# Kernel tuning notes

Measured on AMD Instinct MI355X. Metric: run time of the kernel, lower is better.

The kernel has to match this reference:

```python
import jax, jax.numpy as jnp
import numpy as np

H_MODEL = 1024
N_HEADS = 16
N_KV_HEADS = 4
HEAD_DIM = 64
SLIDING_WINDOW = 512
B, S = 2, 2048
NEG_INF = -1e9


def rotate_half(x):
    half = x.shape[-1] // 2
    return jnp.concatenate([-x[..., half:], x[..., :half]], axis=-1)


def setup_inputs() -> dict:
    key = jax.random.key(0)
    ks = jax.random.split(key, 8)
    hidden_states = jax.random.normal(ks[0], (B, S, H_MODEL), dtype=jnp.float32)
    # RoPE tables (HF style): cos/sin of shape [1, S, head_dim]
    inv_freq = 1.0 / (10000.0 ** (jnp.arange(0, HEAD_DIM, 2, dtype=jnp.float32) / HEAD_DIM))
    pos = jnp.arange(S, dtype=jnp.float32)
    freqs = jnp.einsum('s,d->sd', pos, inv_freq)            # [S, D/2]
    emb = jnp.concatenate([freqs, freqs], axis=-1)          # [S, D]
    cos = jnp.cos(emb)[None]                                # [1, S, D]
    sin = jnp.sin(emb)[None]
    # additive causal + sliding-window mask [1,1,S,S]
    i = jnp.arange(S)[:, None]
    j = jnp.arange(S)[None, :]
    allowed = (j <= i) & (i - j < SLIDING_WINDOW)
    attention_mask = jnp.where(allowed, 0.0, NEG_INF).astype(jnp.float32)[None, None]
    # projection weights (torch Linear stores [out, in]; y = x @ W.T)
    std = 0.02
    Wq = jax.random.normal(ks[1], (N_HEADS * HEAD_DIM, H_MODEL), dtype=jnp.float32) * std
    Wk = jax.random.normal(ks[2], (N_KV_HEADS * HEAD_DIM, H_MODEL), dtype=jnp.float32) * std
    Wv = jax.random.normal(ks[3], (N_KV_HEADS * HEAD_DIM, H_MODEL), dtype=jnp.float32) * std
    Wo = jax.random.normal(ks[4], (H_MODEL, N_HEADS * HEAD_DIM), dtype=jnp.float32) * std
    return {"hidden_states": hidden_states, "cos": cos, "sin": sin,
            "attention_mask": attention_mask, "Wq": Wq, "Wk": Wk, "Wv": Wv, "Wo": Wo}


def reference(hidden_states, cos, sin, attention_mask, Wq, Wk, Wv, Wo):
    b, s, _ = hidden_states.shape
    G = N_HEADS // N_KV_HEADS
    scaling = HEAD_DIM ** -0.5
    # QKV projections -> [B, H, S, D]
    q = jnp.einsum('bsh,oh->bso', hidden_states, Wq).reshape(b, s, N_HEADS, HEAD_DIM).transpose(0, 2, 1, 3)
    k = jnp.einsum('bsh,oh->bso', hidden_states, Wk).reshape(b, s, N_KV_HEADS, HEAD_DIM).transpose(0, 2, 1, 3)
    v = jnp.einsum('bsh,oh->bso', hidden_states, Wv).reshape(b, s, N_KV_HEADS, HEAD_DIM).transpose(0, 2, 1, 3)
    # RoPE (cos/sin broadcast over head dim via unsqueeze(1))
    c = cos[:, None, :, :]
    sn = sin[:, None, :, :]
    q = q * c + rotate_half(q) * sn
    k = k * c + rotate_half(k) * sn
    # GQA eager attention: group query heads over kv heads
    qg = q.reshape(b, N_KV_HEADS, G, s, HEAD_DIM)
    scores = jnp.einsum('bkgqd,bkpd->bkgqp', qg, k) * scaling  # [B,Hkv,G,S,S]
    scores = scores + attention_mask[:, :, None, :, :]
    probs = jax.nn.softmax(scores.astype(jnp.float32), axis=-1).astype(q.dtype)
    out = jnp.einsum('bkgqp,bkpd->bkgqd', probs, v)            # [B,Hkv,G,S,D]
    out = out.reshape(b, N_HEADS, s, HEAD_DIM).transpose(0, 2, 1, 3).reshape(b, s, N_HEADS * HEAD_DIM)
    return jnp.einsum('bso,ho->bsh', out, Wo)
```

## Files before the change

kernel.cpp:

```cpp
#include <hip/hip_runtime.h>
#include <hip/hip_bf16.h>

#define S_LEN 2048
#define NH 16
#define NKV 4
#define HD 64
#define WIN 512
#define BATCH 2

typedef __bf16 bf16_8 __attribute__((ext_vector_type(8)));
typedef __bf16 bf16_4 __attribute__((ext_vector_type(4)));
typedef float f32x4 __attribute__((ext_vector_type(4)));

__device__ inline void gld16(const __bf16* g, __bf16* l) {
    __builtin_amdgcn_global_load_lds(
        (const __attribute__((address_space(1))) void*)g,
        (__attribute__((address_space(3))) void*)l, 16, 0, 0);
}

__global__ __launch_bounds__(256) void cvt5(
    const float* __restrict__ s0, const float* __restrict__ s1,
    const float* __restrict__ s2, const float* __restrict__ s3,
    const float* __restrict__ s4,
    __bf16* __restrict__ d0, __bf16* __restrict__ d1,
    __bf16* __restrict__ d2, __bf16* __restrict__ d3,
    __bf16* __restrict__ d4,
    int c0, int c1, int c2, int c3, int c4)
{
    const int i = blockIdx.x * blockDim.x + threadIdx.x;
    if (i >= c4) return;
    const float* s; __bf16* d; int base;
    if (i < c0)      { s = s0; d = d0; base = 0;  }
    else if (i < c1) { s = s1; d = d1; base = c0; }
    else if (i < c2) { s = s2; d = d2; base = c1; }
    else if (i < c3) { s = s3; d = d3; base = c2; }
    else             { s = s4; d = d4; base = c3; }
    const size_t j = (size_t)(i - base) * 4;
    const f32x4 v = *(const f32x4*)(s + j);
    bf16_4 o;
    o[0] = (__bf16)v[0]; o[1] = (__bf16)v[1];
    o[2] = (__bf16)v[2]; o[3] = (__bf16)v[3];
    *(bf16_4*)(d + j) = o;
}

__global__ __launch_bounds__(256) void gemm_qkv(
    const __bf16* __restrict__ A,
    const __bf16* __restrict__ Wqb,
    const __bf16* __restrict__ Wkb,
    const __bf16* __restrict__ Wvb,
    __bf16* __restrict__ Qb,
    __bf16* __restrict__ Kb,
    __bf16* __restrict__ Vb,
    const float* __restrict__ cosb,
    const float* __restrict__ sinb)
{
    const int K = 1024;
    __shared__ __align__(16) __bf16 As[128 * 32];
    __shared__ __align__(16) __bf16 Bs[128 * 32];

    const int tid  = threadIdx.x;
    const int wave = tid >> 6;
    const int lane = tid & 63;
    const int wr   = wave >> 1;
    const int wc   = wave & 1;

    const int row0 = blockIdx.x * 128;
    const int by   = blockIdx.y;

    const __bf16* B; __bf16* C; int ldc; int col0; bool rope;
    if (by < 8)       { B = Wqb + (size_t)by * 128 * K;        C = Qb; ldc = 1024; col0 = by * 128;        rope = true;  }
    else if (by < 10) { B = Wkb + (size_t)(by - 8) * 128 * K;  C = Kb; ldc = 256;  col0 = (by - 8) * 128;  rope = true;  }
    else              { B = Wvb + (size_t)(by - 10) * 128 * K; C = Vb; ldc = 256;  col0 = (by - 10) * 128; rope = false; }

    const int srow = lane >> 2;
    const int skc  = (lane & 3) << 3;

    const int fm = lane & 15;
    const int fk = (lane >> 4) << 3;

    const f32x4 fzero = {0.f, 0.f, 0.f, 0.f};
    f32x4 acc[4][4];
#pragma unroll
    for (int i = 0; i < 4; ++i)
#pragma unroll
        for (int nt = 0; nt < 4; ++nt) acc[i][nt] = fzero;

    const int ra0 = wave * 16 + srow;
    const int ra1 = 64 + wave * 16 + srow;

    for (int k0 = 0; k0 < K; k0 += 32) {
        gld16(&A[(size_t)(row0 + ra0) * K + k0 + skc], &As[(wave * 16) * 32]);
        gld16(&A[(size_t)(row0 + ra1) * K + k0 + skc], &As[(64 + wave * 16) * 32]);
        gld16(&B[(size_t)ra0 * K + k0 + skc],          &Bs[(wave * 16) * 32]);
        gld16(&B[(size_t)ra1 * K + k0 + skc],          &Bs[(64 + wave * 16) * 32]);
        __syncthreads();

        bf16_8 af[4], bf[4];
#pragma unroll
        for (int i = 0; i < 4; ++i)
            af[i] = *(const bf16_8*)&As[(wr * 64 + i * 16 + fm) * 32 + fk];
#pragma unroll
        for (int nt = 0; nt < 4; ++nt)
            bf[nt] = *(const bf16_8*)&Bs[(wc * 64 + nt * 16 + fm) * 32 + fk];
#pragma unroll
        for (int i = 0; i < 4; ++i)
#pragma unroll
            for (int nt = 0; nt < 4; ++nt)
                acc[i][nt] = __builtin_amdgcn_mfma_f32_16x16x32_bf16(af[i], bf[nt], acc[i][nt], 0, 0, 0);
        __syncthreads();
    }

    const int drow = (lane >> 4) << 2;
    const int cq   = col0 + wc * 64;
#pragma unroll
    for (int i = 0; i < 4; ++i) {
#pragma unroll
        for (int r = 0; r < 4; ++r) {
            const int row = row0 + wr * 64 + i * 16 + drow + r;
            const int s   = row & (S_LEN - 1);
            if (rope) {
#pragma unroll
                for (int nt = 0; nt < 2; ++nt) {
                    const int d = nt * 16 + fm;
                    const float c1 = cosb[s * HD + d];
                    const float s1 = sinb[s * HD + d];
                    const float c2 = cosb[s * HD + d + 32];
                    const float s2 = sinb[s * HD + d + 32];
                    const float x1 = acc[i][nt][r];
                    const float x2 = acc[i][nt + 2][r];
                    C[(size_t)row * ldc + cq + d]      = (__bf16)(x1 * c1 - x2 * s1);
                    C[(size_t)row * ldc + cq + d + 32] = (__bf16)(x2 * c2 + x1 * s2);
                }
            } else {
#pragma unroll
                for (int nt = 0; nt < 4; ++nt)
                    C[(size_t)row * ldc + cq + nt * 16 + fm] = (__bf16)acc[i][nt][r];
            }
        }
    }
}

__global__ __launch_bounds__(256) void gemm_o(
    const __bf16* __restrict__ A,
    const __bf16* __restrict__ B,
    float* __restrict__ C)
{
    const int K = 1024;
    __shared__ __align__(16) __bf16 As[128 * 32];
    __shared__ __align__(16) __bf16 Bs[128 * 32];

    const int tid  = threadIdx.x;
    const int wave = tid >> 6;
    const int lane = tid & 63;
    const int wr   = wave >> 1;
    const int wc   = wave & 1;

    const int row0 = blockIdx.x * 128;
    const int col0 = blockIdx.y * 128;

    const int srow = lane >> 2;
    const int skc  = (lane & 3) << 3;
    const int fm = lane & 15;
    const int fk = (lane >> 4) << 3;

    const f32x4 fzero = {0.f, 0.f, 0.f, 0.f};
    f32x4 acc[4][4];
#pragma unroll
    for (int i = 0; i < 4; ++i)
#pragma unroll
        for (int nt = 0; nt < 4; ++nt) acc[i][nt] = fzero;

    const int ra0 = wave * 16 + srow;
    const int ra1 = 64 + wave * 16 + srow;

    for (int k0 = 0; k0 < K; k0 += 32) {
        gld16(&A[(size_t)(row0 + ra0) * K + k0 + skc], &As[(wave * 16) * 32]);
        gld16(&A[(size_t)(row0 + ra1) * K + k0 + skc], &As[(64 + wave * 16) * 32]);
        gld16(&B[(size_t)(col0 + ra0) * K + k0 + skc], &Bs[(wave * 16) * 32]);
        gld16(&B[(size_t)(col0 + ra1) * K + k0 + skc], &Bs[(64 + wave * 16) * 32]);
        __syncthreads();

        bf16_8 af[4], bf[4];
#pragma unroll
        for (int i = 0; i < 4; ++i)
            af[i] = *(const bf16_8*)&As[(wr * 64 + i * 16 + fm) * 32 + fk];
#pragma unroll
        for (int nt = 0; nt < 4; ++nt)
            bf[nt] = *(const bf16_8*)&Bs[(wc * 64 + nt * 16 + fm) * 32 + fk];
#pragma unroll
        for (int i = 0; i < 4; ++i)
#pragma unroll
            for (int nt = 0; nt < 4; ++nt)
                acc[i][nt] = __builtin_amdgcn_mfma_f32_16x16x32_bf16(af[i], bf[nt], acc[i][nt], 0, 0, 0);
        __syncthreads();
    }

    const int drow = (lane >> 4) << 2;
#pragma unroll
    for (int i = 0; i < 4; ++i)
#pragma unroll
        for (int r = 0; r < 4; ++r) {
            const int row = row0 + wr * 64 + i * 16 + drow + r;
#pragma unroll
            for (int nt = 0; nt < 4; ++nt)
                C[(size_t)row * 1024 + col0 + wc * 64 + nt * 16 + fm] = acc[i][nt][r];
        }
}

__global__ __launch_bounds__(256) void attn_mfma(const __bf16* __restrict__ Q,
                                                 const __bf16* __restrict__ K,
                                                 const __bf16* __restrict__ V,
                                                 __bf16* __restrict__ O)
{
    __shared__ __align__(16) __bf16 Vt[HD][40];
    __shared__ __align__(16) __bf16 Ps[4][16][40];

    const int tid  = threadIdx.x;
    const int wave = tid >> 6;
    const int lane = tid & 63;

    const int qt = blockIdx.x & (S_LEN / 64 - 1);
    const int h  = (blockIdx.x >> 5) & (NH - 1);
    const int b  = blockIdx.x >> 9;
    const int kh = h >> 2;

    const int q0 = qt * 64;
    const int qw = q0 + wave * 16;

    const int fm = lane & 15;
    const int fj = (lane >> 4) << 3;

    const size_t qrow = (size_t)(b * S_LEN + qw + fm) * (NH * HD) + h * HD;
    const bf16_8 qf0 = *(const bf16_8*)&Q[qrow + fj];
    const bf16_8 qf1 = *(const bf16_8*)&Q[qrow + 32 + fj];

    const f32x4 fzero = {0.f, 0.f, 0.f, 0.f};
    f32x4 oacc[4];
    float l[4];
#pragma unroll
    for (int nt = 0; nt < 4; ++nt) oacc[nt] = fzero;
#pragma unroll
    for (int r = 0; r < 4; ++r) l[r] = 0.f;

    const int sj = tid & 31;
    const int sd = (tid >> 5) << 3;

    const int kb_lo = (q0 >= WIN) ? (q0 - WIN) : 0;
    const int qbase = qw + ((lane >> 4) << 2);

    for (int kb = kb_lo; kb <= q0 + 63; kb += 32) {
        __syncthreads();
        {
            bf16_8 vrow = *(const bf16_8*)&V[(size_t)(b * S_LEN + kb + sj) * (NKV * HD) + kh * HD + sd];
#pragma unroll
            for (int u = 0; u < 8; ++u) Vt[sd + u][sj] = vrow[u];
        }
        __syncthreads();

        if (kb <= qw + 15 && (qw - kb) < (WIN + 31)) {
            f32x4 s0 = fzero, s1 = fzero;
            {
                const size_t kr0 = (size_t)(b * S_LEN + kb + fm) * (NKV * HD) + kh * HD;
                const size_t kr1 = (size_t)(b * S_LEN + kb + 16 + fm) * (NKV * HD) + kh * HD;
                bf16_8 k00 = *(const bf16_8*)&K[kr0 + fj];
                bf16_8 k01 = *(const bf16_8*)&K[kr0 + 32 + fj];
                bf16_8 k10 = *(const bf16_8*)&K[kr1 + fj];
                bf16_8 k11 = *(const bf16_8*)&K[kr1 + 32 + fj];
                s0 = __builtin_amdgcn_mfma_f32_16x16x32_bf16(qf0, k00, s0, 0, 0, 0);
                s0 = __builtin_amdgcn_mfma_f32_16x16x32_bf16(qf1, k01, s0, 0, 0, 0);
                s1 = __builtin_amdgcn_mfma_f32_16x16x32_bf16(qf0, k10, s1, 0, 0, 0);
                s1 = __builtin_amdgcn_mfma_f32_16x16x32_bf16(qf1, k11, s1, 0, 0, 0);
            }

            float p0[4], p1[4];
            const int k0i = kb + fm;
            const int k1i = kb + 16 + fm;
#pragma unroll
            for (int r = 0; r < 4; ++r) {
                const int qr = qbase + r;
                const float e0 = __expf(s0[r] * 0.125f);
                const float e1 = __expf(s1[r] * 0.125f);
                p0[r] = (k0i <= qr && qr - k0i < WIN) ? e0 : 0.f;
                p1[r] = (k1i <= qr && qr - k1i < WIN) ? e1 : 0.f;
                l[r] += p0[r] + p1[r];
            }

#pragma unroll
            for (int r = 0; r < 4; ++r) {
                Ps[wave][((lane >> 4) << 2) + r][fm]      = (__bf16)p0[r];
                Ps[wave][((lane >> 4) << 2) + r][16 + fm] = (__bf16)p1[r];
            }

            const bf16_8 pf = *(const bf16_8*)&Ps[wave][fm][fj];
#pragma unroll
            for (int nt = 0; nt < 4; ++nt) {
                const bf16_8 vf = *(const bf16_8*)&Vt[nt * 16 + fm][fj];
                oacc[nt] = __builtin_amdgcn_mfma_f32_16x16x32_bf16(pf, vf, oacc[nt], 0, 0, 0);
            }
        }
    }

#pragma unroll
    for (int off = 8; off > 0; off >>= 1)
#pragma unroll
        for (int r = 0; r < 4; ++r)
            l[r] += __shfl_xor(l[r], off, 64);

    const int drow = (lane >> 4) << 2;
    float inv[4];
#pragma unroll
    for (int r = 0; r < 4; ++r) inv[r] = 1.0f / l[r];
#pragma unroll
    for (int nt = 0; nt < 4; ++nt)
#pragma unroll
        for (int r = 0; r < 4; ++r) {
            const size_t off = (size_t)(b * S_LEN + qw + drow + r) * (NH * HD) + h * HD + nt * 16 + fm;
            O[off] = (__bf16)(oacc[nt][r] * inv[r]);
        }
}

extern "C" void kernel_launch(void* const* d_in, const int* in_sizes, int n_in,
                              void* d_out, int out_size, void* d_ws, size_t ws_size,
                              hipStream_t stream)
{
    const float* hs   = (const float*)d_in[0];
    const float* cosb = (const float*)d_in[1];
    const float* sinb = (const float*)d_in[2];
    const float* Wq = (const float*)d_in[4];
    const float* Wk = (const float*)d_in[5];
    const float* Wv = (const float*)d_in[6];
    const float* Wo = (const float*)d_in[7];

    const int M = BATCH * S_LEN;

    __bf16* hsb = (__bf16*)d_ws;
    __bf16* Ob  = hsb;
    __bf16* Wqb = hsb + (size_t)M * 1024;
    __bf16* Wkb = Wqb + 1024 * 1024;
    __bf16* Wvb = Wkb + 256 * 1024;
    __bf16* Wob = Wvb + 256 * 1024;
    __bf16* Qb  = Wob + 1024 * 1024;
    __bf16* Kb  = Qb  + (size_t)M * 1024;
    __bf16* Vb  = Kb  + (size_t)M * 256;

    const int c0 = 1048576;
    const int c1 = c0 + 262144;
    const int c2 = c1 + 65536;
    const int c3 = c2 + 65536;
    const int c4 = c3 + 262144;

    dim3 blk(256);
    cvt5<<<(c4 + 255) / 256, blk, 0, stream>>>(hs, Wq, Wk, Wv, Wo,
                                               hsb, Wqb, Wkb, Wvb, Wob,
                                               c0, c1, c2, c3, c4);

    gemm_qkv<<<dim3(32, 12), blk, 0, stream>>>(hsb, Wqb, Wkb, Wvb,
                                               Qb, Kb, Vb, cosb, sinb);

    attn_mfma<<<BATCH * NH * (S_LEN / 64), blk, 0, stream>>>(Qb, Kb, Vb, Ob);

    gemm_o<<<dim3(32, 8), blk, 0, stream>>>(Ob, Wob, (float*)d_out);
}
```

Measured before the change: 188.9 us.

## Pre-transpose V in QKV GEMM, drop attention LDS staging, shrink GEMM tiles

The QKV GEMM epilogue now writes V directly in a transposed [b,kv,d,s] layout. The attention kernel then reads V fragments straight from global memory instead of staging and transposing them through shared memory with two block barriers per key step. Each wave also iterates only over its own window-limited key range instead of the block-wide range. The GEMMs switch to 64x128 tiles via a shared macro, doubling grid size for better CU coverage at the cost of less per-block reuse and strided scattered V stores.

```diff
diff --git a/kernel.cpp b/kernel.cpp
--- a/kernel.cpp
+++ b/kernel.cpp
@@ -43,6 +43,47 @@
     *(bf16_4*)(d + j) = o;
 }
 
+#define GEMM_BODY(A_, B_, row0_, colb_)                                        \
+    __shared__ __align__(16) __bf16 As[64 * 32];                               \
+    __shared__ __align__(16) __bf16 Bs[128 * 32];                              \
+    const int tid  = threadIdx.x;                                              \
+    const int wave = tid >> 6;                                                 \
+    const int lane = tid & 63;                                                 \
+    const int wm   = wave & 1;                                                 \
+    const int wn   = wave >> 1;                                                \
+    const int srow = lane >> 2;                                                \
+    const int skc  = (lane & 3) << 3;                                          \
+    const int fm   = lane & 15;                                                \
+    const int fk   = (lane >> 4) << 3;                                         \
+    const f32x4 fzero = {0.f, 0.f, 0.f, 0.f};                                  \
+    f32x4 acc[2][4];                                                           \
+    _Pragma("unroll") for (int i = 0; i < 2; ++i)                              \
+        _Pragma("unroll") for (int nt = 0; nt < 4; ++nt) acc[i][nt] = fzero;   \
+    const int ch0 = wave * 3;                                                  \
+    for (int k0 = 0; k0 < 1024; k0 += 32) {                                    \
+        _Pragma("unroll") for (int t = 0; t < 3; ++t) {                        \
+            const int ch = ch0 + t;                                            \
+            if (ch < 4)                                                        \
+                gld16(&A_[(size_t)(row0_ + ch * 16 + srow) * 1024 + k0 + skc], \
+                      &As[ch * 16 * 32]);                                      \
+            else                                                               \
+                gld16(&B_[(size_t)(colb_ + (ch - 4) * 16 + srow) * 1024 + k0 + skc], \
+                      &Bs[(ch - 4) * 16 * 32]);                                \
+        }                                                                      \
+        __syncthreads();                                                       \
+        bf16_8 af[2], bfr[4];                                                  \
+        _Pragma("unroll") for (int i = 0; i < 2; ++i)                          \
+            af[i] = *(const bf16_8*)&As[(wm * 32 + i * 16 + fm) * 32 + fk];    \
+        _Pragma("unroll") for (int nt = 0; nt < 4; ++nt)                       \
+            bfr[nt] = *(const bf16_8*)&Bs[(wn * 64 + nt * 16 + fm) * 32 + fk]; \
+        _Pragma("unroll") for (int i = 0; i < 2; ++i)                          \
+            _Pragma("unroll") for (int nt = 0; nt < 4; ++nt)                   \
+                acc[i][nt] = __builtin_amdgcn_mfma_f32_16x16x32_bf16(          \
+                    af[i], bfr[nt], acc[i][nt], 0, 0, 0);                      \
+        __syncthreads();                                                       \
+    }                                                                          \
+    const int drow = (lane >> 4) << 2;
+
 __global__ __launch_bounds__(256) void gemm_qkv(
     const __bf16* __restrict__ A,
     const __bf16* __restrict__ Wqb,
@@ -50,75 +91,29 @@
     const __bf16* __restrict__ Wvb,
     __bf16* __restrict__ Qb,
     __bf16* __restrict__ Kb,
-    __bf16* __restrict__ Vb,
+    __bf16* __restrict__ Vt,
     const float* __restrict__ cosb,
     const float* __restrict__ sinb)
 {
-    const int K = 1024;
-    __shared__ __align__(16) __bf16 As[128 * 32];
-    __shared__ __align__(16) __bf16 Bs[128 * 32];
-
-    const int tid  = threadIdx.x;
-    const int wave = tid >> 6;
-    const int lane = tid & 63;
-    const int wr   = wave >> 1;
-    const int wc   = wave & 1;
-
-    const int row0 = blockIdx.x * 128;
+    const int row0 = blockIdx.x * 64;
     const int by   = blockIdx.y;
 
-    const __bf16* B; __bf16* C; int ldc; int col0; bool rope;
-    if (by < 8)       { B = Wqb + (size_t)by * 128 * K;        C = Qb; ldc = 1024; col0 = by * 128;        rope = true;  }
-    else if (by < 10) { B = Wkb + (size_t)(by - 8) * 128 * K;  C = Kb; ldc = 256;  col0 = (by - 8) * 128;  rope = true;  }
-    else              { B = Wvb + (size_t)(by - 10) * 128 * K; C = Vb; ldc = 256;  col0 = (by - 10) * 128; rope = false; }
-
-    const int srow = lane >> 2;
-    const int skc  = (lane & 3) << 3;
-
-    const int fm = lane & 15;
-    const int fk = (lane >> 4) << 3;
-
-    const f32x4 fzero = {0.f, 0.f, 0.f, 0.f};
-    f32x4 acc[4][4];
-#pragma unroll
-    for (int i = 0; i < 4; ++i)
-#pragma unroll
-        for (int nt = 0; nt < 4; ++nt) acc[i][nt] = fzero;
-
-    const int ra0 = wave * 16 + srow;
-    const int ra1 = 64 + wave * 16 + srow;
-
-    for (int k0 = 0; k0 < K; k0 += 32) {
-        gld16(&A[(size_t)(row0 + ra0) * K + k0 + skc], &As[(wave * 16) * 32]);
-        gld16(&A[(size_t)(row0 + ra1) * K + k0 + skc], &As[(64 + wave * 16) * 32]);
-        gld16(&B[(size_t)ra0 * K + k0 + skc],          &Bs[(wave * 16) * 32]);
-        gld16(&B[(size_t)ra1 * K + k0 + skc],          &Bs[(64 + wave * 16) * 32]);
-        __syncthreads();
-
-        bf16_8 af[4], bf[4];
-#pragma unroll
-        for (int i = 0; i < 4; ++i)
-            af[i] = *(const bf16_8*)&As[(wr * 64 + i * 16 + fm) * 32 + fk];
-#pragma unroll
-        for (int nt = 0; nt < 4; ++nt)
-            bf[nt] = *(const bf16_8*)&Bs[(wc * 64 + nt * 16 + fm) * 32 + fk];
-#pragma unroll
-        for (int i = 0; i < 4; ++i)
-#pragma unroll
-            for (int nt = 0; nt < 4; ++nt)
-                acc[i][nt] = __builtin_amdgcn_mfma_f32_16x16x32_bf16(af[i], bf[nt], acc[i][nt], 0, 0, 0);
-        __syncthreads();
-    }
-
-    const int drow = (lane >> 4) << 2;
-    const int cq   = col0 + wc * 64;
-#pragma unroll
-    for (int i = 0; i < 4; ++i) {
-#pragma unroll
-        for (int r = 0; r < 4; ++r) {
-            const int row = row0 + wr * 64 + i * 16 + drow + r;
-            const int s   = row & (S_LEN - 1);
-            if (rope) {
+    const __bf16* B; int colb;
+    __bf16* C; int ldc; int col0; int mode;
+    if (by < 8)       { B = Wqb; colb = by * 128;        C = Qb; ldc = 1024; col0 = by * 128;        mode = 0; }
+    else if (by < 10) { B = Wkb; colb = (by - 8) * 128;  C = Kb; ldc = 256;  col0 = (by - 8) * 128;  mode = 1; }
+    else              { B = Wvb; colb = (by - 10) * 128; C = 0;  ldc = 0;    col0 = (by - 10) * 128; mode = 2; }
+
+    GEMM_BODY(A, (B + (size_t)0), row0, colb)
+
+    const int cq = col0 + wn * 64;
+    if (mode < 2) {
+#pragma unroll
+        for (int i = 0; i < 2; ++i) {
+#pragma unroll
+            for (int r = 0; r < 4; ++r) {
+                const int row = row0 + wm * 32 + i * 16 + drow + r;
+                const int s   = row & (S_LEN - 1);
 #pragma unroll
                 for (int nt = 0; nt < 2; ++nt) {
                     const int d = nt * 16 + fm;
@@ -131,10 +126,22 @@
                     C[(size_t)row * ldc + cq + d]      = (__bf16)(x1 * c1 - x2 * s1);
                     C[(size_t)row * ldc + cq + d + 32] = (__bf16)(x2 * c2 + x1 * s2);
                 }
-            } else {
-#pragma unroll
-                for (int nt = 0; nt < 4; ++nt)
-                    C[(size_t)row * ldc + cq + nt * 16 + fm] = (__bf16)acc[i][nt][r];
+            }
+        }
+    } else {
+        const int kh = cq >> 6;
+#pragma unroll
+        for (int i = 0; i < 2; ++i) {
+#pragma unroll
+            for (int r = 0; r < 4; ++r) {
+                const int row = row0 + wm * 32 + i * 16 + drow + r;
+                const int b   = row >> 11;
+                const int s   = row & (S_LEN - 1);
+#pragma unroll
+                for (int nt = 0; nt < 4; ++nt) {
+                    const int d = nt * 16 + fm;
+                    Vt[(size_t)((b * NKV + kh) * HD + d) * S_LEN + s] = (__bf16)acc[i][nt][r];
+                }
             }
         }
     }
@@ -145,74 +152,27 @@
     const __bf16* __restrict__ B,
     float* __restrict__ C)
 {
-    const int K = 1024;
-    __shared__ __align__(16) __bf16 As[128 * 32];
-    __shared__ __align__(16) __bf16 Bs[128 * 32];
-
-    const int tid  = threadIdx.x;
-    const int wave = tid >> 6;
-    const int lane = tid & 63;
-    const int wr   = wave >> 1;
-    const int wc   = wave & 1;
-
-    const int row0 = blockIdx.x * 128;
-    const int col0 = blockIdx.y * 128;
-
-    const int srow = lane >> 2;
-    const int skc  = (lane & 3) << 3;
-    const int fm = lane & 15;
-    const int fk = (lane >> 4) << 3;
-
-    const f32x4 fzero = {0.f, 0.f, 0.f, 0.f};
-    f32x4 acc[4][4];
-#pragma unroll
-    for (int i = 0; i < 4; ++i)
-#pragma unroll
-        for (int nt = 0; nt < 4; ++nt) acc[i][nt] = fzero;
-
-    const int ra0 = wave * 16 + srow;
-    const int ra1 = 64 + wave * 16 + srow;
-
-    for (int k0 = 0; k0 < K; k0 += 32) {
-        gld16(&A[(size_t)(row0 + ra0) * K + k0 + skc], &As[(wave * 16) * 32]);
-        gld16(&A[(size_t)(row0 + ra1) * K + k0 + skc], &As[(64 + wave * 16) * 32]);
-        gld16(&B[(size_t)(col0 + ra0) * K + k0 + skc], &Bs[(wave * 16) * 32]);
-        gld16(&B[(size_t)(col0 + ra1) * K + k0 + skc], &Bs[(64 + wave * 16) * 32]);
-        __syncthreads();
-
-        bf16_8 af[4], bf[4];
-#pragma unroll
-        for (int i = 0; i < 4; ++i)
-            af[i] = *(const bf16_8*)&As[(wr * 64 + i * 16 + fm) * 32 + fk];
-#pragma unroll
-        for (int nt = 0; nt < 4; ++nt)
-            bf[nt] = *(const bf16_8*)&Bs[(wc * 64 + nt * 16 + fm) * 32 + fk];
-#pragma unroll
-        for (int i = 0; i < 4; ++i)
+    const int row0 = blockIdx.x * 64;
+    const int colb = blockIdx.y * 128;
+
+    GEMM_BODY(A, B, row0, colb)
+
+#pragma unroll
+    for (int i = 0; i < 2; ++i)
+#pragma unroll
+        for (int r = 0; r < 4; ++r) {
+            const int row = row0 + wm * 32 + i * 16 + drow + r;
 #pragma unroll
             for (int nt = 0; nt < 4; ++nt)
-                acc[i][nt] = __builtin_amdgcn_mfma_f32_16x16x32_bf16(af[i], bf[nt], acc[i][nt], 0, 0, 0);
-        __syncthreads();
-    }
-
-    const int drow = (lane >> 4) << 2;
-#pragma unroll
-    for (int i = 0; i < 4; ++i)
-#pragma unroll
-        for (int r = 0; r < 4; ++r) {
-            const int row = row0 + wr * 64 + i * 16 + drow + r;
-#pragma unroll
-            for (int nt = 0; nt < 4; ++nt)
-                C[(size_t)row * 1024 + col0 + wc * 64 + nt * 16 + fm] = acc[i][nt][r];
+                C[(size_t)row * 1024 + colb + wn * 64 + nt * 16 + fm] = acc[i][nt][r];
         }
 }
 
 __global__ __launch_bounds__(256) void attn_mfma(const __bf16* __restrict__ Q,
                                                  const __bf16* __restrict__ K,
-                                                 const __bf16* __restrict__ V,
+                                                 const __bf16* __restrict__ Vt,
                                                  __bf16* __restrict__ O)
 {
-    __shared__ __align__(16) __bf16 Vt[HD][40];
     __shared__ __align__(16) __bf16 Ps[4][16][40];
 
     const int tid  = threadIdx.x;
@@ -224,8 +184,7 @@
     const int b  = blockIdx.x >> 9;
     const int kh = h >> 2;
 
-    const int q0 = qt * 64;
-    const int qw = q0 + wave * 16;
+    const int qw = qt * 64 + wave * 16;
 
     const int fm = lane & 15;
     const int fj = (lane >> 4) << 3;
@@ -242,61 +201,51 @@
 #pragma unroll
     for (int r = 0; r < 4; ++r) l[r] = 0.f;
 
-    const int sj = tid & 31;
-    const int sd = (tid >> 5) << 3;
-
-    const int kb_lo = (q0 >= WIN) ? (q0 - WIN) : 0;
+    const size_t vbase = (size_t)((b * NKV + kh) * HD) * S_LEN;
     const int qbase = qw + ((lane >> 4) << 2);
 
-    for (int kb = kb_lo; kb <= q0 + 63; kb += 32) {
-        __syncthreads();
+    const int lo = (qw >= (WIN - 1)) ? ((qw - WIN + 1) & ~31) : 0;
+    const int hi = (qw + 15) & ~31;
+
+    for (int kb = lo; kb <= hi; kb += 32) {
+        f32x4 s0 = fzero, s1 = fzero;
         {
-            bf16_8 vrow = *(const bf16_8*)&V[(size_t)(b * S_LEN + kb + sj) * (NKV * HD) + kh * HD + sd];
-#pragma unroll
-            for (int u = 0; u < 8; ++u) Vt[sd + u][sj] = vrow[u];
-        }
-        __syncthreads();
-
-        if (kb <= qw + 15 && (qw - kb) < (WIN + 31)) {
-            f32x4 s0 = fzero, s1 = fzero;
-            {
-                const size_t kr0 = (size_t)(b * S_LEN + kb + fm) * (NKV * HD) + kh * HD;
-                const size_t kr1 = (size_t)(b * S_LEN + kb + 16 + fm) * (NKV * HD) + kh * HD;
-                bf16_8 k00 = *(const bf16_8*)&K[kr0 + fj];
-                bf16_8 k01 = *(const bf16_8*)&K[kr0 + 32 + fj];
-                bf16_8 k10 = *(const bf16_8*)&K[kr1 + fj];
-                bf16_8 k11 = *(const bf16_8*)&K[kr1 + 32 + fj];
-                s0 = __builtin_amdgcn_mfma_f32_16x16x32_bf16(qf0, k00, s0, 0, 0, 0);
-                s0 = __builtin_amdgcn_mfma_f32_16x16x32_bf16(qf1, k01, s0, 0, 0, 0);
-                s1 = __builtin_amdgcn_mfma_f32_16x16x32_bf16(qf0, k10, s1, 0, 0, 0);
-                s1 = __builtin_amdgcn_mfma_f32_16x16x32_bf16(qf1, k11, s1, 0, 0, 0);
-            }
-
-            float p0[4], p1[4];
-            const int k0i = kb + fm;
-            const int k1i = kb + 16 + fm;
-#pragma unroll
-            for (int r = 0; r < 4; ++r) {
-                const int qr = qbase + r;
-                const float e0 = __expf(s0[r] * 0.125f);
-                const float e1 = __expf(s1[r] * 0.125f);
-                p0[r] = (k0i <= qr && qr - k0i < WIN) ? e0 : 0.f;
-                p1[r] = (k1i <= qr && qr - k1i < WIN) ? e1 : 0.f;
-                l[r] += p0[r] + p1[r];
-            }
-
-#pragma unroll
-            for (int r = 0; r < 4; ++r) {
-                Ps[wave][((lane >> 4) << 2) + r][fm]      = (__bf16)p0[r];
-                Ps[wave][((lane >> 4) << 2) + r][16 + fm] = (__bf16)p1[r];
-            }
-
-            const bf16_8 pf = *(const bf16_8*)&Ps[wave][fm][fj];
-#pragma unroll
-            for (int nt = 0; nt < 4; ++nt) {
-                const bf16_8 vf = *(const bf16_8*)&Vt[nt * 16 + fm][fj];
-                oacc[nt] = __builtin_amdgcn_mfma_f32_16x16x32_bf16(pf, vf, oacc[nt], 0, 0, 0);
-            }
+            const size_t kr0 = (size_t)(b * S_LEN + kb + fm) * (NKV * HD) + kh * HD;
+            const size_t kr1 = (size_t)(b * S_LEN + kb + 16 + fm) * (NKV * HD) + kh * HD;
+            bf16_8 k00 = *(const bf16_8*)&K[kr0 + fj];
+            bf16_8 k01 = *(const bf16_8*)&K[kr0 + 32 + fj];
+            bf16_8 k10 = *(const bf16_8*)&K[kr1 + fj];
+            bf16_8 k11 = *(const bf16_8*)&K[kr1 + 32 + fj];
+            s0 = __builtin_amdgcn_mfma_f32_16x16x32_bf16(qf0, k00, s0, 0, 0, 0);
+            s0 = __builtin_amdgcn_mfma_f32_16x16x32_bf16(qf1, k01, s0, 0, 0, 0);
+            s1 = __builtin_amdgcn_mfma_f32_16x16x32_bf16(qf0, k10, s1, 0, 0, 0);
+            s1 = __builtin_amdgcn_mfma_f32_16x16x32_bf16(qf1, k11, s1, 0, 0, 0);
+        }
+
+        float p0[4], p1[4];
+        const int k0i = kb + fm;
+        const int k1i = kb + 16 + fm;
+#pragma unroll
+        for (int r = 0; r < 4; ++r) {
+            const int qr = qbase + r;
+            const float e0 = __expf(s0[r] * 0.125f);
+            const float e1 = __expf(s1[r] * 0.125f);
+            p0[r] = (k0i <= qr && qr - k0i < WIN) ? e0 : 0.f;
+            p1[r] = (k1i <= qr && qr - k1i < WIN) ? e1 : 0.f;
+            l[r] += p0[r] + p1[r];
+        }
+
+#pragma unroll
+        for (int r = 0; r < 4; ++r) {
+            Ps[wave][((lane >> 4) << 2) + r][fm]      = (__bf16)p0[r];
+            Ps[wave][((lane >> 4) << 2) + r][16 + fm] = (__bf16)p1[r];
+        }
+
+        const bf16_8 pf = *(const bf16_8*)&Ps[wave][fm][fj];
+#pragma unroll
+        for (int nt = 0; nt < 4; ++nt) {
+            const bf16_8 vf = *(const bf16_8*)&Vt[vbase + (size_t)(nt * 16 + fm) * S_LEN + kb + fj];
+            oacc[nt] = __builtin_amdgcn_mfma_f32_16x16x32_bf16(pf, vf, oacc[nt], 0, 0, 0);
         }
     }
 
@@ -341,7 +290,7 @@
     __bf16* Wob = Wvb + 256 * 1024;
     __bf16* Qb  = Wob + 1024 * 1024;
     __bf16* Kb  = Qb  + (size_t)M * 1024;
-    __bf16* Vb  = Kb  + (size_t)M * 256;
+    __bf16* Vtb = Kb  + (size_t)M * 256;
 
     const int c0 = 1048576;
     const int c1 = c0 + 262144;
@@ -354,10 +303,10 @@
                                                hsb, Wqb, Wkb, Wvb, Wob,
                                                c0, c1, c2, c3, c4);
 
-    gemm_qkv<<<dim3(32, 12), blk, 0, stream>>>(hsb, Wqb, Wkb, Wvb,
-                                               Qb, Kb, Vb, cosb, sinb);
-
-    attn_mfma<<<BATCH * NH * (S_LEN / 64), blk, 0, stream>>>(Qb, Kb, Vb, Ob);
-
-    gemm_o<<<dim3(32, 8), blk, 0, stream>>>(Ob, Wob, (float*)d_out);
-}
+    gemm_qkv<<<dim3(64, 12), blk, 0, stream>>>(hsb, Wqb, Wkb, Wvb,
+                                               Qb, Kb, Vtb, cosb, sinb);
+
+    attn_mfma<<<BATCH * NH * (S_LEN / 64), blk, 0, stream>>>(Qb, Kb, Vtb, Ob);
+
+    gemm_o<<<dim3(64, 8), blk, 0, stream>>>(Ob, Wob, (float*)d_out);
+}
```

Result: slower. 202.8 us (+7.3%).
